# Performance work log

Hardware: AMD Instinct MI355X
Metric: run time of the kernel (lower is better)

Reference implementation:

```python
import jax, jax.numpy as jnp
import numpy as np

ALPHA = 0.2      # leaky_alpha
GRAPH_ITR = 2    # graph_itr
ENC_LEN = 250    # output_begin_idx = encoder_sequence.shape[1]


def _char_embedding(ids, emb, conv_w, conv_b):
    # ids: [B,N,Wl] int -> char-CNN: embed, conv1d over word dim, relu, max-pool
    x = emb[ids]                                      # [B,N,Wl,E]
    B, N, Wl, E = x.shape
    x = x.reshape(B * N, Wl, E).transpose(0, 2, 1)    # [B*N, E, Wl]
    y = jax.lax.conv_general_dilated(x, conv_w, (1,), [(2, 2)],
                                     dimension_numbers=('NCH', 'OIH', 'NCH'))
    y = jax.nn.relu(y + conv_b[None, :, None])        # [B*N, F, Wl]
    return y.max(axis=2).reshape(B, N, -1)            # [B,N,F]


def _dynamic_graph(x, W0a, W0b, b0, W1, b1, Wout, bout):
    # Pairwise MLP on concat(x_i, x_j); first layer computed as split matmuls
    # so the [B,N,N,2d] concat is never materialized.
    hi = jnp.einsum('bnd,de->bne', x, W0a)            # [B,N,d]
    hj = jnp.einsum('bnd,de->bne', x, W0b)            # [B,N,d]
    h = jax.nn.relu(hi[:, :, None, :] + hj[:, None, :, :] + b0)   # [B,N,N,d]
    h = jax.nn.relu(jnp.einsum('bnme,ef->bnmf', h, W1) + b1)      # [B,N,N,d]
    return jax.nn.sigmoid(jnp.einsum('bnme,e->bnm', h, Wout[:, 0]) + bout[0])


def _gat(x, adj, W, a1, a2):
    # Multi-head GAT: per-head projection, additive attention, adjacency-masked softmax.
    Wh = jnp.einsum('bnd,hdk->bhnk', x, W)            # [B,H,N,hid]
    f1 = jnp.einsum('bhnk,hk->bhn', Wh, a1)
    f2 = jnp.einsum('bhnk,hk->bhn', Wh, a2)
    e = jax.nn.leaky_relu(f1[:, :, :, None] + f2[:, :, None, :], ALPHA)  # [B,H,N,N]
    e = jnp.where(adj[:, None, :, :] > 0, e, -9e15)
    attn = jax.nn.softmax(e, axis=-1)
    h = jax.nn.elu(jnp.einsum('bhnm,bhmk->bhnk', attn, Wh))
    B, H, N, K = h.shape
    return h.transpose(0, 2, 1, 3).reshape(B, N, H * K)  # concat heads -> [B,N,d]


def setup_inputs() -> dict:
    key = jax.random.key(0)
    ks = jax.random.split(key, 20)
    B, Le, Ld, Wl = 2, 250, 150, 16
    Vin, E, F, K = 128, 64, 128, 5
    H, hid, Vout = 8, 32, 5000
    d = H * hid  # 256
    s = lambda k, sh: jax.random.normal(k, sh, dtype=jnp.float32) * 0.05
    return {
        'encoder_sequence': jax.random.randint(ks[0], (B, Le, Wl), 0, Vin),
        'initial_decoder_sequence': jax.random.randint(ks[1], (B, Ld, Wl), 0, Vin),
        'fixed_graph': jax.random.randint(ks[2], (B, Le + Ld, Le + Ld), 0, 2),
        'char_emb': s(ks[3], (Vin, E)),
        'conv_w': s(ks[4], (F, E, K)),
        'conv_b': jnp.zeros((F,), jnp.float32),
        'hst_W': s(ks[5], (F, d)),
        'hst_b': jnp.zeros((d,), jnp.float32),
        'dg_W0a': s(ks[6], (d, d)),
        'dg_W0b': s(ks[7], (d, d)),
        'dg_b0': jnp.zeros((d,), jnp.float32),
        'dg_W1': s(ks[8], (d, d)),
        'dg_b1': jnp.zeros((d,), jnp.float32),
        'dg_Wout': s(ks[9], (d, 1)),
        'dg_bout': jnp.zeros((1,), jnp.float32),
        'att_W': s(ks[10], (H, d, hid)),
        'att_a1': s(ks[11], (H, hid)),
        'att_a2': s(ks[12], (H, hid)),
        'out_W': s(ks[13], (d, Vout)),
        'out_b': jnp.zeros((Vout,), jnp.float32),
    }


def reference(encoder_sequence, initial_decoder_sequence, fixed_graph,
              char_emb, conv_w, conv_b, hst_W, hst_b,
              dg_W0a, dg_W0b, dg_b0, dg_W1, dg_b1, dg_Wout, dg_bout,
              att_W, att_a1, att_a2, out_W, out_b):
    ids = jnp.concatenate([encoder_sequence, initial_decoder_sequence], axis=1)  # [B,N,Wl]
    x = _char_embedding(ids, char_emb, conv_w, conv_b)    # [B,N,F]
    x = x @ hst_W + hst_b                                 # [B,N,d]
    fixed = fixed_graph.astype(jnp.float32)
    for _ in range(GRAPH_ITR):
        dyn = _dynamic_graph(x, dg_W0a, dg_W0b, dg_b0, dg_W1, dg_b1, dg_Wout, dg_bout)
        adj = jnp.clip(dyn + fixed, 0.0, 1.0)             # combine dynamic + fixed graph
        x = _gat(x, adj, att_W, att_a1, att_a2)
    return x[:, ENC_LEN:, :] @ out_W + out_b              # [B, dec_len, Vout]
```

## Files before the change

kernel.cpp:

```cpp
#include <hip/hip_runtime.h>
#include <hip/hip_bf16.h>
#include <math.h>


__device__ __forceinline__ float bf2f_raw(unsigned int u) {
    union { unsigned int i; float f; } cv; cv.i = u << 16; return cv.f;
}
__device__ __forceinline__ unsigned short f2bf(float f) {
    __hip_bfloat16 h = __float2bfloat16(f);
    return *reinterpret_cast<unsigned short*>(&h);
}

__global__ __launch_bounds__(256) void k_prep(const float* emb, const float* convw,
                                              float* T, const float* W,
                                              unsigned short* Wb) {
    int bid = blockIdx.x, t = threadIdx.x;
    if (bid < 128) {
        int v = bid;
        __shared__ float er[64];
        if (t < 64) er[t] = emb[v * 64 + t];
        __syncthreads();
        if (t < 128) {
            float acc[5] = {0.f, 0.f, 0.f, 0.f, 0.f};
            const float* w = convw + t * 320;
            for (int e = 0; e < 64; ++e) {
                float xe = er[e];
#pragma unroll
                for (int k = 0; k < 5; ++k) acc[k] += xe * w[e * 5 + k];
            }
#pragma unroll
            for (int k = 0; k < 5; ++k) T[(k * 128 + v) * 128 + t] = acc[k];
        }
    } else {
        int i0 = (bid - 128) * 512 + t * 2;
        if (i0 < 256 * 5000) {
            float2 w2 = *reinterpret_cast<const float2*>(W + i0);
            unsigned int u = ((unsigned int)f2bf(w2.y) << 16) | f2bf(w2.x);
            *reinterpret_cast<unsigned int*>(Wb + i0) = u;
        }
    }
}

__global__ __launch_bounds__(256) void k_convhst(const int* enc, const int* dec,
                                                 const float* convb, const float* T,
                                                 const float* hstW, const float* hstb,
                                                 float* x) {
    int w0 = blockIdx.x * 2, t = threadIdx.x;
    __shared__ int ids[2][16];
    __shared__ float xcl[2][128];
    if (t < 32) {
        int r = t >> 4, c = t & 15;
        int w = w0 + r;
        int b = w / 400, n = w % 400;
        ids[r][c] = (n < 250) ? enc[(b * 250 + n) * 16 + c]
                              : dec[(b * 150 + (n - 250)) * 16 + c];
    }
    __syncthreads();
    {
        int r = t >> 7, f = t & 127;
        float best = -1e30f;
        for (int p = 0; p < 16; ++p) {
            float s = 0.f;
#pragma unroll
            for (int k = 0; k < 5; ++k) {
                int q = p + k - 2;
                if (q >= 0 && q < 16) s += T[(k * 128 + ids[r][q]) * 128 + f];
            }
            best = fmaxf(best, s);
        }
        xcl[r][f] = fmaxf(best + convb[f], 0.f);
    }
    __syncthreads();
    float acc0 = hstb[t], acc1 = acc0;
    for (int c = 0; c < 128; ++c) {
        float wv = hstW[c * 256 + t];
        acc0 += xcl[0][c] * wv;
        acc1 += xcl[1][c] * wv;
    }
    x[w0 * 256 + t] = acc0;
    x[(w0 + 1) * 256 + t] = acc1;
}

__global__ __launch_bounds__(256) void k_wh(const float* x, const float* attW,
                                            const float* a1g, const float* a2g,
                                            float* Wh, float* f1, float* f2) {
    int blk = blockIdx.x, t = threadIdx.x;
    int w0 = blk * 2;
    int h = t >> 5, k = t & 31;
    __shared__ float xr[2][256];
    for (int i = t; i < 512; i += 256) xr[i >> 8][i & 255] = x[w0 * 256 + i];
    __syncthreads();
    float acc0 = 0.f, acc1 = 0.f;
    const float* Wp = attW + h * 8192 + k;
#pragma unroll 8
    for (int d = 0; d < 256; ++d) {
        float wv = Wp[d * 32];
        acc0 += xr[0][d] * wv;
        acc1 += xr[1][d] * wv;
    }
    float a1v = a1g[t], a2v = a2g[t];
    int b = w0 / 400;
    int bh = b * 8 + h;
    float accs[2] = {acc0, acc1};
#pragma unroll
    for (int rw = 0; rw < 2; ++rw) {
        int n = (w0 + rw) % 400;
        Wh[(bh * 400 + n) * 32 + k] = accs[rw];
        float v1 = accs[rw] * a1v, v2 = accs[rw] * a2v;
#pragma unroll
        for (int mm = 16; mm >= 1; mm >>= 1) {
            v1 += __shfl_xor(v1, mm, 64);
            v2 += __shfl_xor(v2, mm, 64);
        }
        if (k == 0) { f1[bh * 400 + n] = v1; f2[bh * 400 + n] = v2; }
    }
}

__global__ __launch_bounds__(256) void k_attn(const float* Wh, const float* f1g,
                                              const float* f2g, float* xout) {
    int tile = blockIdx.x, bh = blockIdx.y;
    int b = bh >> 3, h = bh & 7;
    int t = threadIdx.x;
    int n0 = tile * 8;
    __shared__ float f2l[400];
    __shared__ float4 plT[400];
    __shared__ float f1l[8];
    __shared__ float red[4][8][4][4];
    __shared__ float sred[2][4][4];
    __shared__ float wmax[4];

    float fm = -1e30f;
    for (int m = t; m < 400; m += 256) {
        float v = f2g[bh * 400 + m];
        f2l[m] = v;
        fm = fmaxf(fm, v);
    }
    if (t < 8) f1l[t] = f1g[bh * 400 + n0 + t];
#pragma unroll
    for (int mm = 32; mm >= 1; mm >>= 1) fm = fmaxf(fm, __shfl_xor(fm, mm, 64));
    if ((t & 63) == 0) wmax[t >> 6] = fm;
    __syncthreads();
    float fmax2 = fmaxf(fmaxf(wmax[0], wmax[1]), fmaxf(wmax[2], wmax[3]));

    int g = t & 7, kq = (t >> 3) & 7, wv = t >> 6;
    int gm = g + 8 * wv;
    const float4* WhG = (const float4*)(Wh + bh * 12800);
    for (int it = 0; it < 2; ++it) {
        float f1a = f1l[it * 4 + 0], f1b = f1l[it * 4 + 1];
        float f1c = f1l[it * 4 + 2], f1d = f1l[it * 4 + 3];
        float rm0 = f1a + fmax2; rm0 = rm0 > 0.f ? rm0 : 0.2f * rm0;
        float rm1 = f1b + fmax2; rm1 = rm1 > 0.f ? rm1 : 0.2f * rm1;
        float rm2 = f1c + fmax2; rm2 = rm2 > 0.f ? rm2 : 0.2f * rm2;
        float rm3 = f1d + fmax2; rm3 = rm3 > 0.f ? rm3 : 0.2f * rm3;
        float ps0 = 0.f, ps1 = 0.f, ps2 = 0.f, ps3 = 0.f;
        for (int m = t; m < 400; m += 256) {
            float f2v = f2l[m];
            float e0 = f1a + f2v; e0 = e0 > 0.f ? e0 : 0.2f * e0;
            float e1 = f1b + f2v; e1 = e1 > 0.f ? e1 : 0.2f * e1;
            float e2 = f1c + f2v; e2 = e2 > 0.f ? e2 : 0.2f * e2;
            float e3 = f1d + f2v; e3 = e3 > 0.f ? e3 : 0.2f * e3;
            float4 pv;
            pv.x = __expf(e0 - rm0); ps0 += pv.x;
            pv.y = __expf(e1 - rm1); ps1 += pv.y;
            pv.z = __expf(e2 - rm2); ps2 += pv.z;
            pv.w = __expf(e3 - rm3); ps3 += pv.w;
            plT[m] = pv;
        }
        {
            float v0 = ps0, v1 = ps1, v2 = ps2, v3 = ps3;
#pragma unroll
            for (int mm = 32; mm >= 1; mm >>= 1) {
                v0 += __shfl_xor(v0, mm, 64);
                v1 += __shfl_xor(v1, mm, 64);
                v2 += __shfl_xor(v2, mm, 64);
                v3 += __shfl_xor(v3, mm, 64);
            }
            if ((t & 63) == 0) {
                int wq = t >> 6;
                sred[it & 1][0][wq] = v0; sred[it & 1][1][wq] = v1;
                sred[it & 1][2][wq] = v2; sred[it & 1][3][wq] = v3;
            }
        }
        __syncthreads();
        float a[4][4];
#pragma unroll
        for (int rr = 0; rr < 4; ++rr)
#pragma unroll
            for (int c = 0; c < 4; ++c) a[rr][c] = 0.f;
#pragma unroll 4
        for (int m = gm; m < 400; m += 32) {
            float4 w4 = WhG[m * 8 + kq];
            float4 p4 = plT[m];
            a[0][0] += p4.x * w4.x; a[0][1] += p4.x * w4.y; a[0][2] += p4.x * w4.z; a[0][3] += p4.x * w4.w;
            a[1][0] += p4.y * w4.x; a[1][1] += p4.y * w4.y; a[1][2] += p4.y * w4.z; a[1][3] += p4.y * w4.w;
            a[2][0] += p4.z * w4.x; a[2][1] += p4.z * w4.y; a[2][2] += p4.z * w4.z; a[2][3] += p4.z * w4.w;
            a[3][0] += p4.w * w4.x; a[3][1] += p4.w * w4.y; a[3][2] += p4.w * w4.z; a[3][3] += p4.w * w4.w;
        }
#pragma unroll
        for (int rr = 0; rr < 4; ++rr)
#pragma unroll
            for (int c = 0; c < 4; ++c) {
                float v = a[rr][c];
                v += __shfl_xor(v, 1, 64);
                v += __shfl_xor(v, 2, 64);
                v += __shfl_xor(v, 4, 64);
                a[rr][c] = v;
            }
        if (g == 0) {
#pragma unroll
            for (int rr = 0; rr < 4; ++rr)
#pragma unroll
                for (int c = 0; c < 4; ++c) red[wv][kq][rr][c] = a[rr][c];
        }
        __syncthreads();
        if (t < 128) {
            int rw3 = t >> 5, kk = t & 31;
            int q3 = kk >> 2, c3 = kk & 3;
            float s = sred[it & 1][rw3][0] + sred[it & 1][rw3][1]
                    + sred[it & 1][rw3][2] + sred[it & 1][rw3][3];
            float o = (red[0][q3][rw3][c3] + red[1][q3][rw3][c3]
                     + red[2][q3][rw3][c3] + red[3][q3][rw3][c3]) / s;
            o = o > 0.f ? o : (__expf(o) - 1.f);
            int n = n0 + it * 4 + rw3;
            xout[(b * 400 + n) * 256 + h * 32 + kk] = o;
        }
    }
}

__global__ __launch_bounds__(256) void k_out(const float* x, const unsigned short* Wb,
                                             const float* bias, float* out) {
    int vt = blockIdx.x, rg = blockIdx.y, t = threadIdx.x;
    __shared__ float xr[6][256];
    int r0 = rg * 6;
    int b = r0 / 150, n0 = 250 + (r0 % 150);
    for (int i = t; i < 1536; i += 256) {
        int rr = i >> 8, dd = i & 255;
        xr[rr][dd] = x[(b * 400 + n0 + rr) * 256 + dd];
    }
    __syncthreads();
    int v = vt * 512 + t * 2;
    if (v >= 5000) return;
    float acc[6][2];
#pragma unroll
    for (int rr = 0; rr < 6; ++rr) { acc[rr][0] = 0.f; acc[rr][1] = 0.f; }
    const unsigned short* Wp = Wb + v;
#pragma unroll 8
    for (int dd = 0; dd < 256; ++dd) {
        unsigned int wu = *reinterpret_cast<const unsigned int*>(Wp + dd * 5000);
        float w0 = bf2f_raw(wu & 0xFFFFu);
        float w1 = bf2f_raw(wu >> 16);
#pragma unroll
        for (int rr = 0; rr < 6; ++rr) {
            float xv = xr[rr][dd];
            acc[rr][0] += xv * w0;
            acc[rr][1] += xv * w1;
        }
    }
    float b0 = bias[v], b1 = bias[v + 1];
#pragma unroll
    for (int rr = 0; rr < 6; ++rr) {
        out[(r0 + rr) * 5000 + v]     = acc[rr][0] + b0;
        out[(r0 + rr) * 5000 + v + 1] = acc[rr][1] + b1;
    }
}

extern "C" void kernel_launch(void* const* d_in, const int* in_sizes, int n_in,
                              void* d_out, int out_size, void* d_ws, size_t ws_size,
                              hipStream_t stream) {
    const int*   enc   = (const int*)d_in[0];
    const int*   dec   = (const int*)d_in[1];
    const float* emb   = (const float*)d_in[3];
    const float* convw = (const float*)d_in[4];
    const float* convb = (const float*)d_in[5];
    const float* hstW  = (const float*)d_in[6];
    const float* hstb  = (const float*)d_in[7];
    const float* attW  = (const float*)d_in[15];
    const float* a1    = (const float*)d_in[16];
    const float* a2    = (const float*)d_in[17];
    const float* outW  = (const float*)d_in[18];
    const float* outb  = (const float*)d_in[19];
    float* out = (float*)d_out;

    char* ws = (char*)d_ws;
    float* T   = (float*)ws; ws += 5 * 128 * 128 * 4;
    float* xA  = (float*)ws; ws += 800 * 256 * 4;
    float* xB  = (float*)ws; ws += 800 * 256 * 4;
    float* Wh  = (float*)ws; ws += 16 * 400 * 32 * 4;
    float* f1  = (float*)ws; ws += 16 * 400 * 4;
    float* f2  = (float*)ws; ws += 16 * 400 * 4;
    unsigned short* Wb = (unsigned short*)ws; ws += 256 * 5000 * 2;

    k_prep<<<2628, 256, 0, stream>>>(emb, convw, T, outW, Wb);
    k_convhst<<<400, 256, 0, stream>>>(enc, dec, convb, T, hstW, hstb, xA);

    float* xin = xA;
    float* xo  = xB;
    for (int it = 0; it < 2; ++it) {
        k_wh<<<400, 256, 0, stream>>>(xin, attW, a1, a2, Wh, f1, f2);
        k_attn<<<dim3(50, 16), 256, 0, stream>>>(Wh, f1, f2, xo);
        float* tmp = xin; xin = xo; xo = tmp;
    }
    k_out<<<dim3(10, 50), 256, 0, stream>>>(xin, Wb, outb, out);
}
```

Baseline: 101.3 us.

## Fuse GAT stages across kernels and compute only decoder rows in final attention

Fuses the char-conv/hst projection with the first Wh projection, and the first attention with the second Wh projection, so the node features x no longer round-trip through global memory. The final attention layer runs only for the 150 decoder rows per batch that the output projection consumes. The kernel count drops from seven to five. In exchange, each fused attention block now recomputes the f2 staging and row max for all 8 heads, and the attention loop uses a different per-warp split over heads and rows.

```diff
diff --git a/kernel.cpp b/kernel.cpp
--- a/kernel.cpp
+++ b/kernel.cpp
@@ -10,6 +10,7 @@
     __hip_bfloat16 h = __float2bfloat16(f);
     return *reinterpret_cast<unsigned short*>(&h);
 }
+__device__ __forceinline__ float leaky(float e) { return e > 0.f ? e : 0.2f * e; }
 
 __global__ __launch_bounds__(256) void k_prep(const float* emb, const float* convw,
                                               float* T, const float* W,
@@ -41,17 +42,19 @@
     }
 }
 
-__global__ __launch_bounds__(256) void k_convhst(const int* enc, const int* dec,
-                                                 const float* convb, const float* T,
-                                                 const float* hstW, const float* hstb,
-                                                 float* x) {
+__global__ __launch_bounds__(256) void k_convwh(const int* enc, const int* dec,
+                                                const float* convb, const float* T,
+                                                const float* hstW, const float* hstb,
+                                                const float* attW,
+                                                const float* a1g, const float* a2g,
+                                                float* Wh, float* f1, float* f2) {
     int w0 = blockIdx.x * 2, t = threadIdx.x;
     __shared__ int ids[2][16];
     __shared__ float xcl[2][128];
+    __shared__ float x0[2][256];
     if (t < 32) {
         int r = t >> 4, c = t & 15;
-        int w = w0 + r;
-        int b = w / 400, n = w % 400;
+        int w = w0 + r, b = w / 400, n = w % 400;
         ids[r][c] = (n < 250) ? enc[(b * 250 + n) * 16 + c]
                               : dec[(b * 150 + (n - 250)) * 16 + c];
     }
@@ -71,32 +74,25 @@
         xcl[r][f] = fmaxf(best + convb[f], 0.f);
     }
     __syncthreads();
-    float acc0 = hstb[t], acc1 = acc0;
-    for (int c = 0; c < 128; ++c) {
-        float wv = hstW[c * 256 + t];
-        acc0 += xcl[0][c] * wv;
-        acc1 += xcl[1][c] * wv;
-    }
-    x[w0 * 256 + t] = acc0;
-    x[(w0 + 1) * 256 + t] = acc1;
-}
-
-__global__ __launch_bounds__(256) void k_wh(const float* x, const float* attW,
-                                            const float* a1g, const float* a2g,
-                                            float* Wh, float* f1, float* f2) {
-    int blk = blockIdx.x, t = threadIdx.x;
-    int w0 = blk * 2;
+    {
+        float acc0 = hstb[t], acc1 = acc0;
+        for (int c = 0; c < 128; ++c) {
+            float wv = hstW[c * 256 + t];
+            acc0 += xcl[0][c] * wv;
+            acc1 += xcl[1][c] * wv;
+        }
+        x0[0][t] = acc0;
+        x0[1][t] = acc1;
+    }
+    __syncthreads();
     int h = t >> 5, k = t & 31;
-    __shared__ float xr[2][256];
-    for (int i = t; i < 512; i += 256) xr[i >> 8][i & 255] = x[w0 * 256 + i];
-    __syncthreads();
     float acc0 = 0.f, acc1 = 0.f;
     const float* Wp = attW + h * 8192 + k;
 #pragma unroll 8
     for (int d = 0; d < 256; ++d) {
         float wv = Wp[d * 32];
-        acc0 += xr[0][d] * wv;
-        acc1 += xr[1][d] * wv;
+        acc0 += x0[0][d] * wv;
+        acc1 += x0[1][d] * wv;
     }
     float a1v = a1g[t], a2v = a2g[t];
     int b = w0 / 400;
@@ -116,113 +112,150 @@
     }
 }
 
-__global__ __launch_bounds__(256) void k_attn(const float* Wh, const float* f1g,
-                                              const float* f2g, float* xout) {
-    int tile = blockIdx.x, bh = blockIdx.y;
-    int b = bh >> 3, h = bh & 7;
-    int t = threadIdx.x;
-    int n0 = tile * 8;
-    __shared__ float f2l[400];
-    __shared__ float4 plT[400];
+__global__ __launch_bounds__(256) void k_attnwh(const float* WhI, const float* f1I,
+                                                const float* f2I, const float* attW,
+                                                const float* a1g, const float* a2g,
+                                                float* WhO, float* f1O, float* f2O) {
+    int w0 = blockIdx.x * 2, t = threadIdx.x;
+    int b = w0 / 400, n0 = w0 % 400;
+    __shared__ float f2l[8][400];
+    __shared__ float x1[2][256];
+    __shared__ float f1l[8][2];
+    __shared__ float fmax2[8];
+    for (int h = 0; h < 8; ++h)
+        for (int m = t; m < 400; m += 256)
+            f2l[h][m] = f2I[(b * 8 + h) * 400 + m];
+    if (t < 16) f1l[t >> 1][t & 1] = f1I[(b * 8 + (t >> 1)) * 400 + n0 + (t & 1)];
+    __syncthreads();
+    int wv = t >> 6, lane = t & 63;
+    {
+        int h = wv * 2 + (lane >> 5), mm0 = lane & 31;
+        float fm = -1e30f;
+        for (int m = mm0; m < 400; m += 32) fm = fmaxf(fm, f2l[h][m]);
+#pragma unroll
+        for (int s = 16; s >= 1; s >>= 1) fm = fmaxf(fm, __shfl_xor(fm, s, 64));
+        if (mm0 == 0) fmax2[h] = fm;
+    }
+    __syncthreads();
+    int g = t & 7, kq = (t >> 3) & 7;
+    for (int hh = 0; hh < 2; ++hh) {
+        int h = wv * 2 + hh;
+        int bh = b * 8 + h;
+        float f1a = f1l[h][0], f1b = f1l[h][1];
+        float rm0 = leaky(f1a + fmax2[h]);
+        float rm1 = leaky(f1b + fmax2[h]);
+        float a0[4] = {0.f, 0.f, 0.f, 0.f}, a1r[4] = {0.f, 0.f, 0.f, 0.f};
+        float ps0 = 0.f, ps1 = 0.f;
+        const float4* WhG = (const float4*)(WhI + bh * 12800);
+        for (int m = g; m < 400; m += 8) {
+            float4 w4 = WhG[m * 8 + kq];
+            float f2v = f2l[h][m];
+            float p0 = __expf(leaky(f1a + f2v) - rm0); ps0 += p0;
+            float p1 = __expf(leaky(f1b + f2v) - rm1); ps1 += p1;
+            a0[0] += p0 * w4.x; a0[1] += p0 * w4.y; a0[2] += p0 * w4.z; a0[3] += p0 * w4.w;
+            a1r[0] += p1 * w4.x; a1r[1] += p1 * w4.y; a1r[2] += p1 * w4.z; a1r[3] += p1 * w4.w;
+        }
+#pragma unroll
+        for (int s = 4; s >= 1; s >>= 1) {
+            ps0 += __shfl_xor(ps0, s, 64);
+            ps1 += __shfl_xor(ps1, s, 64);
+#pragma unroll
+            for (int c = 0; c < 4; ++c) {
+                a0[c] += __shfl_xor(a0[c], s, 64);
+                a1r[c] += __shfl_xor(a1r[c], s, 64);
+            }
+        }
+        if (g == 0) {
+            float4 o0, o1;
+            float* p0v = &o0.x; float* p1v = &o1.x;
+#pragma unroll
+            for (int c = 0; c < 4; ++c) {
+                float v0 = a0[c] / ps0; p0v[c] = v0 > 0.f ? v0 : (__expf(v0) - 1.f);
+                float v1 = a1r[c] / ps1; p1v[c] = v1 > 0.f ? v1 : (__expf(v1) - 1.f);
+            }
+            *(float4*)&x1[0][h * 32 + kq * 4] = o0;
+            *(float4*)&x1[1][h * 32 + kq * 4] = o1;
+        }
+    }
+    __syncthreads();
+    int h = t >> 5, k = t & 31;
+    float acc0 = 0.f, acc1 = 0.f;
+    const float* Wp = attW + h * 8192 + k;
+#pragma unroll 8
+    for (int d = 0; d < 256; ++d) {
+        float wv2 = Wp[d * 32];
+        acc0 += x1[0][d] * wv2;
+        acc1 += x1[1][d] * wv2;
+    }
+    float a1v = a1g[t], a2v = a2g[t];
+    int bh = b * 8 + h;
+    float accs[2] = {acc0, acc1};
+#pragma unroll
+    for (int rw = 0; rw < 2; ++rw) {
+        int n = n0 + rw;
+        WhO[(bh * 400 + n) * 32 + k] = accs[rw];
+        float v1 = accs[rw] * a1v, v2 = accs[rw] * a2v;
+#pragma unroll
+        for (int mm = 16; mm >= 1; mm >>= 1) {
+            v1 += __shfl_xor(v1, mm, 64);
+            v2 += __shfl_xor(v2, mm, 64);
+        }
+        if (k == 0) { f1O[bh * 400 + n] = v1; f2O[bh * 400 + n] = v2; }
+    }
+}
+
+__global__ __launch_bounds__(256) void k_attn2(const float* WhI, const float* f1I,
+                                               const float* f2I, float* xout) {
+    int bid = blockIdx.x, t = threadIdx.x;
+    int b = bid / 150, n = 250 + (bid % 150);
+    __shared__ float f2l[8][400];
     __shared__ float f1l[8];
-    __shared__ float red[4][8][4][4];
-    __shared__ float sred[2][4][4];
-    __shared__ float wmax[4];
-
-    float fm = -1e30f;
-    for (int m = t; m < 400; m += 256) {
-        float v = f2g[bh * 400 + m];
-        f2l[m] = v;
-        fm = fmaxf(fm, v);
-    }
-    if (t < 8) f1l[t] = f1g[bh * 400 + n0 + t];
-#pragma unroll
-    for (int mm = 32; mm >= 1; mm >>= 1) fm = fmaxf(fm, __shfl_xor(fm, mm, 64));
-    if ((t & 63) == 0) wmax[t >> 6] = fm;
-    __syncthreads();
-    float fmax2 = fmaxf(fmaxf(wmax[0], wmax[1]), fmaxf(wmax[2], wmax[3]));
-
-    int g = t & 7, kq = (t >> 3) & 7, wv = t >> 6;
-    int gm = g + 8 * wv;
-    const float4* WhG = (const float4*)(Wh + bh * 12800);
-    for (int it = 0; it < 2; ++it) {
-        float f1a = f1l[it * 4 + 0], f1b = f1l[it * 4 + 1];
-        float f1c = f1l[it * 4 + 2], f1d = f1l[it * 4 + 3];
-        float rm0 = f1a + fmax2; rm0 = rm0 > 0.f ? rm0 : 0.2f * rm0;
-        float rm1 = f1b + fmax2; rm1 = rm1 > 0.f ? rm1 : 0.2f * rm1;
-        float rm2 = f1c + fmax2; rm2 = rm2 > 0.f ? rm2 : 0.2f * rm2;
-        float rm3 = f1d + fmax2; rm3 = rm3 > 0.f ? rm3 : 0.2f * rm3;
-        float ps0 = 0.f, ps1 = 0.f, ps2 = 0.f, ps3 = 0.f;
-        for (int m = t; m < 400; m += 256) {
-            float f2v = f2l[m];
-            float e0 = f1a + f2v; e0 = e0 > 0.f ? e0 : 0.2f * e0;
-            float e1 = f1b + f2v; e1 = e1 > 0.f ? e1 : 0.2f * e1;
-            float e2 = f1c + f2v; e2 = e2 > 0.f ? e2 : 0.2f * e2;
-            float e3 = f1d + f2v; e3 = e3 > 0.f ? e3 : 0.2f * e3;
-            float4 pv;
-            pv.x = __expf(e0 - rm0); ps0 += pv.x;
-            pv.y = __expf(e1 - rm1); ps1 += pv.y;
-            pv.z = __expf(e2 - rm2); ps2 += pv.z;
-            pv.w = __expf(e3 - rm3); ps3 += pv.w;
-            plT[m] = pv;
-        }
-        {
-            float v0 = ps0, v1 = ps1, v2 = ps2, v3 = ps3;
-#pragma unroll
-            for (int mm = 32; mm >= 1; mm >>= 1) {
-                v0 += __shfl_xor(v0, mm, 64);
-                v1 += __shfl_xor(v1, mm, 64);
-                v2 += __shfl_xor(v2, mm, 64);
-                v3 += __shfl_xor(v3, mm, 64);
-            }
-            if ((t & 63) == 0) {
-                int wq = t >> 6;
-                sred[it & 1][0][wq] = v0; sred[it & 1][1][wq] = v1;
-                sred[it & 1][2][wq] = v2; sred[it & 1][3][wq] = v3;
-            }
-        }
-        __syncthreads();
-        float a[4][4];
-#pragma unroll
-        for (int rr = 0; rr < 4; ++rr)
-#pragma unroll
-            for (int c = 0; c < 4; ++c) a[rr][c] = 0.f;
-#pragma unroll 4
-        for (int m = gm; m < 400; m += 32) {
+    __shared__ float fmax2[8];
+    for (int h = 0; h < 8; ++h)
+        for (int m = t; m < 400; m += 256)
+            f2l[h][m] = f2I[(b * 8 + h) * 400 + m];
+    if (t < 8) f1l[t] = f1I[(b * 8 + t) * 400 + n];
+    __syncthreads();
+    int wv = t >> 6, lane = t & 63;
+    {
+        int h = wv * 2 + (lane >> 5), mm0 = lane & 31;
+        float fm = -1e30f;
+        for (int m = mm0; m < 400; m += 32) fm = fmaxf(fm, f2l[h][m]);
+#pragma unroll
+        for (int s = 16; s >= 1; s >>= 1) fm = fmaxf(fm, __shfl_xor(fm, s, 64));
+        if (mm0 == 0) fmax2[h] = fm;
+    }
+    __syncthreads();
+    int g = t & 7, kq = (t >> 3) & 7;
+    for (int hh = 0; hh < 2; ++hh) {
+        int h = wv * 2 + hh;
+        int bh = b * 8 + h;
+        float f1n = f1l[h];
+        float rm = leaky(f1n + fmax2[h]);
+        float a0[4] = {0.f, 0.f, 0.f, 0.f};
+        float ps = 0.f;
+        const float4* WhG = (const float4*)(WhI + bh * 12800);
+        for (int m = g; m < 400; m += 8) {
             float4 w4 = WhG[m * 8 + kq];
-            float4 p4 = plT[m];
-            a[0][0] += p4.x * w4.x; a[0][1] += p4.x * w4.y; a[0][2] += p4.x * w4.z; a[0][3] += p4.x * w4.w;
-            a[1][0] += p4.y * w4.x; a[1][1] += p4.y * w4.y; a[1][2] += p4.y * w4.z; a[1][3] += p4.y * w4.w;
-            a[2][0] += p4.z * w4.x; a[2][1] += p4.z * w4.y; a[2][2] += p4.z * w4.z; a[2][3] += p4.z * w4.w;
-            a[3][0] += p4.w * w4.x; a[3][1] += p4.w * w4.y; a[3][2] += p4.w * w4.z; a[3][3] += p4.w * w4.w;
-        }
-#pragma unroll
-        for (int rr = 0; rr < 4; ++rr)
+            float p = __expf(leaky(f1n + f2l[h][m]) - rm);
+            ps += p;
+            a0[0] += p * w4.x; a0[1] += p * w4.y; a0[2] += p * w4.z; a0[3] += p * w4.w;
+        }
+#pragma unroll
+        for (int s = 4; s >= 1; s >>= 1) {
+            ps += __shfl_xor(ps, s, 64);
+#pragma unroll
+            for (int c = 0; c < 4; ++c) a0[c] += __shfl_xor(a0[c], s, 64);
+        }
+        if (g == 0) {
+            float4 o;
+            float* ov = &o.x;
 #pragma unroll
             for (int c = 0; c < 4; ++c) {
-                float v = a[rr][c];
-                v += __shfl_xor(v, 1, 64);
-                v += __shfl_xor(v, 2, 64);
-                v += __shfl_xor(v, 4, 64);
-                a[rr][c] = v;
-            }
-        if (g == 0) {
-#pragma unroll
-            for (int rr = 0; rr < 4; ++rr)
-#pragma unroll
-                for (int c = 0; c < 4; ++c) red[wv][kq][rr][c] = a[rr][c];
-        }
-        __syncthreads();
-        if (t < 128) {
-            int rw3 = t >> 5, kk = t & 31;
-            int q3 = kk >> 2, c3 = kk & 3;
-            float s = sred[it & 1][rw3][0] + sred[it & 1][rw3][1]
-                    + sred[it & 1][rw3][2] + sred[it & 1][rw3][3];
-            float o = (red[0][q3][rw3][c3] + red[1][q3][rw3][c3]
-                     + red[2][q3][rw3][c3] + red[3][q3][rw3][c3]) / s;
-            o = o > 0.f ? o : (__expf(o) - 1.f);
-            int n = n0 + it * 4 + rw3;
-            xout[(b * 400 + n) * 256 + h * 32 + kk] = o;
+                float v = a0[c] / ps;
+                ov[c] = v > 0.f ? v : (__expf(v) - 1.f);
+            }
+            *(float4*)&xout[(b * 400 + n) * 256 + h * 32 + kq * 4] = o;
         }
     }
 }
@@ -282,23 +315,21 @@
     float* out = (float*)d_out;
 
     char* ws = (char*)d_ws;
-    float* T   = (float*)ws; ws += 5 * 128 * 128 * 4;
-    float* xA  = (float*)ws; ws += 800 * 256 * 4;
-    float* xB  = (float*)ws; ws += 800 * 256 * 4;
-    float* Wh  = (float*)ws; ws += 16 * 400 * 32 * 4;
-    float* f1  = (float*)ws; ws += 16 * 400 * 4;
-    float* f2  = (float*)ws; ws += 16 * 400 * 4;
+    float* T    = (float*)ws; ws += 5 * 128 * 128 * 4;
+    float* WhA  = (float*)ws; ws += 16 * 400 * 32 * 4;
+    float* WhB  = (float*)ws; ws += 16 * 400 * 32 * 4;
+    float* f1A  = (float*)ws; ws += 16 * 400 * 4;
+    float* f2A  = (float*)ws; ws += 16 * 400 * 4;
+    float* f1B  = (float*)ws; ws += 16 * 400 * 4;
+    float* f2B  = (float*)ws; ws += 16 * 400 * 4;
+    float* x2   = (float*)ws; ws += 800 * 256 * 4;
     unsigned short* Wb = (unsigned short*)ws; ws += 256 * 5000 * 2;
 
     k_prep<<<2628, 256, 0, stream>>>(emb, convw, T, outW, Wb);
-    k_convhst<<<400, 256, 0, stream>>>(enc, dec, convb, T, hstW, hstb, xA);
-
-    float* xin = xA;
-    float* xo  = xB;
-    for (int it = 0; it < 2; ++it) {
-        k_wh<<<400, 256, 0, stream>>>(xin, attW, a1, a2, Wh, f1, f2);
-        k_attn<<<dim3(50, 16), 256, 0, stream>>>(Wh, f1, f2, xo);
-        float* tmp = xin; xin = xo; xo = tmp;
-    }
-    k_out<<<dim3(10, 50), 256, 0, stream>>>(xin, Wb, outb, out);
-}
+    k_convwh<<<400, 256, 0, stream>>>(enc, dec, convb, T, hstW, hstb, attW,
+                                      a1, a2, WhA, f1A, f2A);
+    k_attnwh<<<400, 256, 0, stream>>>(WhA, f1A, f2A, attW, a1, a2,
+                                      WhB, f1B, f2B);
+    k_attn2<<<300, 256, 0, stream>>>(WhB, f1B, f2B, x2);
+    k_out<<<dim3(10, 50), 256, 0, stream>>>(x2, Wb, outb, out);
+}
```

Result: slower. 136.8 us (+35.1%).

## Fuse char-CNN with first GAT projection and restrict final attention to decoder rows

Applied to the files above, without the earlier changes.

Merges the conv/hst kernel with the first Wh/f1/f2 projection so the intermediate x never goes through global memory, removing one launch. The second attention pass now covers only rows 250..399, the only ones the output projection reads, with n_base offsetting tiles and clamping the tail row. An extra barrier is added at the end of each attention iteration to guard shared-memory reuse, and the separate Wh/f buffers avoid aliasing.

```diff
diff --git a/kernel.cpp b/kernel.cpp
--- a/kernel.cpp
+++ b/kernel.cpp
@@ -41,17 +41,19 @@
     }
 }
 
-__global__ __launch_bounds__(256) void k_convhst(const int* enc, const int* dec,
-                                                 const float* convb, const float* T,
-                                                 const float* hstW, const float* hstb,
-                                                 float* x) {
+__global__ __launch_bounds__(256) void k_convwh(const int* enc, const int* dec,
+                                                const float* convb, const float* T,
+                                                const float* hstW, const float* hstb,
+                                                const float* attW,
+                                                const float* a1g, const float* a2g,
+                                                float* Wh, float* f1, float* f2) {
     int w0 = blockIdx.x * 2, t = threadIdx.x;
     __shared__ int ids[2][16];
     __shared__ float xcl[2][128];
+    __shared__ float x0[2][256];
     if (t < 32) {
         int r = t >> 4, c = t & 15;
-        int w = w0 + r;
-        int b = w / 400, n = w % 400;
+        int w = w0 + r, b = w / 400, n = w % 400;
         ids[r][c] = (n < 250) ? enc[(b * 250 + n) * 16 + c]
                               : dec[(b * 150 + (n - 250)) * 16 + c];
     }
@@ -71,14 +73,42 @@
         xcl[r][f] = fmaxf(best + convb[f], 0.f);
     }
     __syncthreads();
-    float acc0 = hstb[t], acc1 = acc0;
-    for (int c = 0; c < 128; ++c) {
-        float wv = hstW[c * 256 + t];
-        acc0 += xcl[0][c] * wv;
-        acc1 += xcl[1][c] * wv;
-    }
-    x[w0 * 256 + t] = acc0;
-    x[(w0 + 1) * 256 + t] = acc1;
+    {
+        float acc0 = hstb[t], acc1 = acc0;
+        for (int c = 0; c < 128; ++c) {
+            float wv = hstW[c * 256 + t];
+            acc0 += xcl[0][c] * wv;
+            acc1 += xcl[1][c] * wv;
+        }
+        x0[0][t] = acc0;
+        x0[1][t] = acc1;
+    }
+    __syncthreads();
+    int h = t >> 5, k = t & 31;
+    float acc0 = 0.f, acc1 = 0.f;
+    const float* Wp = attW + h * 8192 + k;
+#pragma unroll 8
+    for (int d = 0; d < 256; ++d) {
+        float wv = Wp[d * 32];
+        acc0 += x0[0][d] * wv;
+        acc1 += x0[1][d] * wv;
+    }
+    float a1v = a1g[t], a2v = a2g[t];
+    int b = w0 / 400;
+    int bh = b * 8 + h;
+    float accs[2] = {acc0, acc1};
+#pragma unroll
+    for (int rw = 0; rw < 2; ++rw) {
+        int n = (w0 + rw) % 400;
+        Wh[(bh * 400 + n) * 32 + k] = accs[rw];
+        float v1 = accs[rw] * a1v, v2 = accs[rw] * a2v;
+#pragma unroll
+        for (int mm = 16; mm >= 1; mm >>= 1) {
+            v1 += __shfl_xor(v1, mm, 64);
+            v2 += __shfl_xor(v2, mm, 64);
+        }
+        if (k == 0) { f1[bh * 400 + n] = v1; f2[bh * 400 + n] = v2; }
+    }
 }
 
 __global__ __launch_bounds__(256) void k_wh(const float* x, const float* attW,
@@ -117,11 +147,12 @@
 }
 
 __global__ __launch_bounds__(256) void k_attn(const float* Wh, const float* f1g,
-                                              const float* f2g, float* xout) {
+                                              const float* f2g, float* xout,
+                                              int n_base) {
     int tile = blockIdx.x, bh = blockIdx.y;
     int b = bh >> 3, h = bh & 7;
     int t = threadIdx.x;
-    int n0 = tile * 8;
+    int n0 = n_base + tile * 8;
     __shared__ float f2l[400];
     __shared__ float4 plT[400];
     __shared__ float f1l[8];
@@ -135,7 +166,10 @@
         f2l[m] = v;
         fm = fmaxf(fm, v);
     }
-    if (t < 8) f1l[t] = f1g[bh * 400 + n0 + t];
+    if (t < 8) {
+        int n = n0 + t; if (n > 399) n = 399;
+        f1l[t] = f1g[bh * 400 + n];
+    }
 #pragma unroll
     for (int mm = 32; mm >= 1; mm >>= 1) fm = fmaxf(fm, __shfl_xor(fm, mm, 64));
     if ((t & 63) == 0) wmax[t >> 6] = fm;
@@ -166,20 +200,17 @@
             pv.w = __expf(e3 - rm3); ps3 += pv.w;
             plT[m] = pv;
         }
-        {
-            float v0 = ps0, v1 = ps1, v2 = ps2, v3 = ps3;
-#pragma unroll
-            for (int mm = 32; mm >= 1; mm >>= 1) {
-                v0 += __shfl_xor(v0, mm, 64);
-                v1 += __shfl_xor(v1, mm, 64);
-                v2 += __shfl_xor(v2, mm, 64);
-                v3 += __shfl_xor(v3, mm, 64);
-            }
-            if ((t & 63) == 0) {
-                int wq = t >> 6;
-                sred[it & 1][0][wq] = v0; sred[it & 1][1][wq] = v1;
-                sred[it & 1][2][wq] = v2; sred[it & 1][3][wq] = v3;
-            }
+#pragma unroll
+        for (int mm = 32; mm >= 1; mm >>= 1) {
+            ps0 += __shfl_xor(ps0, mm, 64);
+            ps1 += __shfl_xor(ps1, mm, 64);
+            ps2 += __shfl_xor(ps2, mm, 64);
+            ps3 += __shfl_xor(ps3, mm, 64);
+        }
+        if ((t & 63) == 0) {
+            int wq = t >> 6;
+            sred[it & 1][0][wq] = ps0; sred[it & 1][1][wq] = ps1;
+            sred[it & 1][2][wq] = ps2; sred[it & 1][3][wq] = ps3;
         }
         __syncthreads();
         float a[4][4];
@@ -222,8 +253,10 @@
                      + red[2][q3][rw3][c3] + red[3][q3][rw3][c3]) / s;
             o = o > 0.f ? o : (__expf(o) - 1.f);
             int n = n0 + it * 4 + rw3;
+            if (n > 399) n = 399;
             xout[(b * 400 + n) * 256 + h * 32 + kk] = o;
         }
+        __syncthreads();
     }
 }
 
@@ -282,23 +315,22 @@
     float* out = (float*)d_out;
 
     char* ws = (char*)d_ws;
-    float* T   = (float*)ws; ws += 5 * 128 * 128 * 4;
-    float* xA  = (float*)ws; ws += 800 * 256 * 4;
-    float* xB  = (float*)ws; ws += 800 * 256 * 4;
-    float* Wh  = (float*)ws; ws += 16 * 400 * 32 * 4;
-    float* f1  = (float*)ws; ws += 16 * 400 * 4;
-    float* f2  = (float*)ws; ws += 16 * 400 * 4;
+    float* T    = (float*)ws; ws += 5 * 128 * 128 * 4;
+    float* WhA  = (float*)ws; ws += 16 * 400 * 32 * 4;
+    float* WhB  = (float*)ws; ws += 16 * 400 * 32 * 4;
+    float* f1A  = (float*)ws; ws += 16 * 400 * 4;
+    float* f2A  = (float*)ws; ws += 16 * 400 * 4;
+    float* f1B  = (float*)ws; ws += 16 * 400 * 4;
+    float* f2B  = (float*)ws; ws += 16 * 400 * 4;
+    float* x1   = (float*)ws; ws += 800 * 256 * 4;
+    float* x2   = (float*)ws; ws += 800 * 256 * 4;
     unsigned short* Wb = (unsigned short*)ws; ws += 256 * 5000 * 2;
 
     k_prep<<<2628, 256, 0, stream>>>(emb, convw, T, outW, Wb);
-    k_convhst<<<400, 256, 0, stream>>>(enc, dec, convb, T, hstW, hstb, xA);
-
-    float* xin = xA;
-    float* xo  = xB;
-    for (int it = 0; it < 2; ++it) {
-        k_wh<<<400, 256, 0, stream>>>(xin, attW, a1, a2, Wh, f1, f2);
-        k_attn<<<dim3(50, 16), 256, 0, stream>>>(Wh, f1, f2, xo);
-        float* tmp = xin; xin = xo; xo = tmp;
-    }
-    k_out<<<dim3(10, 50), 256, 0, stream>>>(xin, Wb, outb, out);
-}
+    k_convwh<<<400, 256, 0, stream>>>(enc, dec, convb, T, hstW, hstb, attW,
+                                      a1, a2, WhA, f1A, f2A);
+    k_attn<<<dim3(50, 16), 256, 0, stream>>>(WhA, f1A, f2A, x1, 0);
+    k_wh<<<400, 256, 0, stream>>>(x1, attW, a1, a2, WhB, f1B, f2B);
+    k_attn<<<dim3(19, 16), 256, 0, stream>>>(WhB, f1B, f2B, x2, 250);
+    k_out<<<dim3(10, 50), 256, 0, stream>>>(x2, Wb, outb, out);
+}
```

Result: faster. 95.39 us, median of 2 (-5.8%).
